# Performance work log

Measured on AMD Instinct MI355X. Metric: run time of the kernel, lower is better.

Reference implementation:

```python
import jax, jax.numpy as jnp
import numpy as np

N_NODES = 50000
N_EDGES = 800000
D_MODEL = 128
N_HEADS = 4
N_LAYERS = 2
F_HEAD = D_MODEL // N_HEADS


def setup_inputs() -> dict:
    key = jax.random.key(0)
    ks = jax.random.split(key, 6)
    x = jax.random.normal(ks[0], (N_NODES, D_MODEL), dtype=jnp.float32)
    edge_index = jax.random.randint(ks[1], (2, N_EDGES), 0, N_NODES, dtype=jnp.int64)
    scale = 1.0 / np.sqrt(D_MODEL)
    W = jax.random.normal(ks[2], (N_LAYERS, D_MODEL, D_MODEL), dtype=jnp.float32) * scale
    a_src = jax.random.normal(ks[3], (N_LAYERS, N_HEADS, F_HEAD), dtype=jnp.float32) * scale
    a_dst = jax.random.normal(ks[4], (N_LAYERS, N_HEADS, F_HEAD), dtype=jnp.float32) * scale
    b = jnp.zeros((N_LAYERS, D_MODEL), dtype=jnp.float32)
    return {"x": x, "edge_index": edge_index, "W": W, "a_src": a_src, "a_dst": a_dst, "b": b}


def _gat_layer(x, src, dst, W_l, a_src_l, a_dst_l, b_l, apply_act):
    N = x.shape[0]
    H, F = a_src_l.shape
    # projected node features, split into heads: [N, H, F]
    h = (x @ W_l).reshape(N, H, F)
    # per-node attention contributions: [N, H]
    alpha_s = jnp.einsum("nhf,hf->nh", h, a_src_l)
    alpha_d = jnp.einsum("nhf,hf->nh", h, a_dst_l)
    # per-edge raw scores, LeakyReLU(0.2): [E, H]
    e = jax.nn.leaky_relu(alpha_s[src] + alpha_d[dst], negative_slope=0.2)
    # numerically-stable segment softmax over edges grouped by target node
    e_max = jax.ops.segment_max(e, dst, num_segments=N)
    e_exp = jnp.exp(e - e_max[dst])
    denom = jax.ops.segment_sum(e_exp, dst, num_segments=N)
    alpha = e_exp / (denom[dst] + 1e-16)  # [E, H]
    # gather source features, weight, scatter-add to targets
    msg = h[src] * alpha[:, :, None]  # [E, H, F]
    out = jax.ops.segment_sum(msg, dst, num_segments=N).reshape(N, H * F)
    out = out + x + b_l  # skip connection (dims match) + bias
    return jax.nn.elu(out) if apply_act else out


def reference(x, edge_index, W, a_src, a_dst, b):
    src, dst = edge_index[0], edge_index[1]
    L = W.shape[0]
    for l in range(L):
        x = _gat_layer(x, src, dst, W[l], a_src[l], a_dst[l], b[l], apply_act=(l < L - 1))
    return x
```

## Files before the change

### kernel.cpp

```cpp
#include <hip/hip_runtime.h>
#include <math.h>

constexpr int NN = 50000;
constexpr int NE = 800000;
constexpr int D  = 128;
constexpr int NH = 4;
constexpr int NBUK = (NN + 255) / 256;
constexpr int CAP  = 4608;

typedef __attribute__((ext_vector_type(8))) short short8v;
typedef __attribute__((ext_vector_type(4))) float f32x4;

__device__ inline unsigned short rne_bf16(float f) {
    unsigned bits = __float_as_uint(f);
    return (unsigned short)((bits + 0x7FFFu + ((bits >> 16) & 1u)) >> 16);
}

__global__ __launch_bounds__(256) void partition_kernel(
    const int* __restrict__ src, const int* __restrict__ dst,
    int* __restrict__ bwp, unsigned* __restrict__ bukbuf)
{
    __shared__ int cnt[NBUK];
    __shared__ int run[NBUK];
    for (int i = threadIdx.x; i < NBUK; i += 256) cnt[i] = 0;
    __syncthreads();
    const int base = blockIdx.x * 2048;
    int s_[8], b_[8], dl_[8];
    #pragma unroll
    for (int i = 0; i < 8; ++i) {
        int e = base + i * 256 + threadIdx.x;
        bool ok = (e < NE);
        s_[i] = ok ? src[e] : 0;
        int d = ok ? dst[e] : 0;
        b_[i] = d >> 8; dl_[i] = d & 255;
        if (ok) atomicAdd(&cnt[b_[i]], 1);
    }
    __syncthreads();
    for (int i = threadIdx.x; i < NBUK; i += 256)
        run[i] = cnt[i] ? atomicAdd(&bwp[i], cnt[i]) : 0;
    __syncthreads();
    #pragma unroll
    for (int i = 0; i < 8; ++i) {
        int e = base + i * 256 + threadIdx.x;
        if (e < NE) {
            int pos = atomicAdd(&run[b_[i]], 1);
            if (pos < CAP)
                bukbuf[b_[i] * CAP + pos] = (unsigned)s_[i] | ((unsigned)dl_[i] << 16);
        }
    }
}

__global__ __launch_bounds__(256) void bucket_sort_kernel(
    const unsigned* __restrict__ bukbuf, const int* __restrict__ bwp,
    int* __restrict__ row_start, int* __restrict__ row_end,
    unsigned short* __restrict__ srcs)
{
    const int b = blockIdx.x;
    const int t = threadIdx.x;
    const int cnt = min(bwp[b], CAP);
    const int base = b * CAP;
    __shared__ int hist[256];
    __shared__ int run[256];
    __shared__ int s[256];
    __shared__ unsigned short stage[CAP];
    hist[t] = 0;
    __syncthreads();
    for (int i = t; i < cnt; i += 256)
        atomicAdd(&hist[bukbuf[base + i] >> 16], 1);
    __syncthreads();
    int v = hist[t];
    s[t] = v;
    __syncthreads();
    for (int off = 1; off < 256; off <<= 1) {
        int u = (t >= off) ? s[t - off] : 0;
        __syncthreads();
        s[t] += u;
        __syncthreads();
    }
    const int excl = s[t] - v;
    const int node = b * 256 + t;
    if (node < NN) {
        row_start[node] = base + excl;
        row_end[node]   = base + excl + v;
    }
    run[t] = excl;
    __syncthreads();
    for (int i = t; i < cnt; i += 256) {
        unsigned p = bukbuf[base + i];
        int pos = atomicAdd(&run[p >> 16], 1);
        stage[pos] = (unsigned short)(p & 0xFFFFu);
    }
    __syncthreads();
    for (int i = t; i < cnt; i += 256) srcs[base + i] = stage[i];
}

__global__ __launch_bounds__(256) void repack_kernel(const float* __restrict__ W,
                                                     unsigned short* __restrict__ Wpk,
                                                     int* __restrict__ bwp) {
    if (blockIdx.x == 0 && threadIdx.x < NBUK) bwp[threadIdx.x] = 0;
    int tid = blockIdx.x * 256 + threadIdx.x;
    if (tid >= 2 * 2048) return;
    int layer = tid >> 11;
    int rest  = tid & 2047;
    int tile  = rest >> 8;
    int kstep = (rest >> 6) & 3;
    int lane  = rest & 63;
    int col   = tile * 16 + (lane & 15);
    int kbase = kstep * 32 + (lane >> 4) * 8;
    const float* Wl = W + (size_t)layer * D * D;
    unsigned short v[8];
    #pragma unroll
    for (int j = 0; j < 8; ++j) v[j] = rne_bf16(Wl[(kbase + j) * D + col]);
    *(uint4*)(Wpk + (size_t)tid * 8) = *(const uint4*)v;
}

template<int BF16IN>
__global__ __launch_bounds__(256) void gemm_alpha_kernel(
    const void* __restrict__ xin, const unsigned short* __restrict__ Wpk,
    const float* __restrict__ a_src, const float* __restrict__ a_dst,
    unsigned short* __restrict__ hb, float* __restrict__ alpha_s,
    float* __restrict__ alpha_d)
{
    __shared__ unsigned short xl[64 * 128];
    const int t = threadIdx.x;
    const int row0 = blockIdx.x * 64;

    if constexpr (BF16IN) {
        const unsigned short* xb = (const unsigned short*)xin;
        #pragma unroll
        for (int it = 0; it < 4; ++it) {
            int idx = it * 256 + t;
            int r   = idx >> 4;
            int c8  = (idx & 15) * 8;
            int n   = row0 + r;
            uint4 v = {0u, 0u, 0u, 0u};
            if (n < NN) v = *(const uint4*)(xb + (size_t)n * D + c8);
            *(uint4*)(xl + r * 128 + (c8 ^ ((r & 7) << 3))) = v;
        }
    } else {
        const float* xf = (const float*)xin;
        #pragma unroll
        for (int it = 0; it < 8; ++it) {
            int idx = it * 256 + t;
            int r   = idx >> 5;
            int c4  = (idx & 31) * 4;
            int n   = row0 + r;
            float4 v;
            if (n < NN) v = *(const float4*)(xf + (size_t)n * D + c4);
            else { v.x = 0.f; v.y = 0.f; v.z = 0.f; v.w = 0.f; }
            unsigned p0 = ((unsigned)rne_bf16(v.y) << 16) | rne_bf16(v.x);
            unsigned p1 = ((unsigned)rne_bf16(v.w) << 16) | rne_bf16(v.z);
            uint2 pv; pv.x = p0; pv.y = p1;
            *(uint2*)(xl + r * 128 + (c4 ^ ((r & 7) << 3))) = pv;
        }
    }
    __syncthreads();

    const int wv  = t >> 6;
    const int l   = t & 63;
    const int l15 = l & 15;
    const int g   = l >> 4;
    const int strip = wv * 16;
    const int arow  = strip + l15;

    f32x4 acc[8];
    #pragma unroll
    for (int i = 0; i < 8; ++i) acc[i] = (f32x4){0.f, 0.f, 0.f, 0.f};

    #pragma unroll
    for (int ks = 0; ks < 4; ++ks) {
        const int k0 = ks * 32 + g * 8;
        short8v a = *(const short8v*)(xl + arow * 128 + (k0 ^ ((arow & 7) << 3)));
        #pragma unroll
        for (int tl = 0; tl < 8; ++tl) {
            short8v b = *(const short8v*)(Wpk + ((size_t)(tl * 4 + ks) * 64 + l) * 8);
            acc[tl] = __builtin_amdgcn_mfma_f32_16x16x32_bf16(a, b, acc[tl], 0, 0, 0);
        }
    }

    float as_t[8], ad_t[8];
    #pragma unroll
    for (int tl = 0; tl < 8; ++tl) {
        as_t[tl] = a_src[tl * 16 + l15];
        ad_t[tl] = a_dst[tl * 16 + l15];
    }

    #pragma unroll
    for (int r = 0; r < 4; ++r) {
        const int n = row0 + strip + g * 4 + r;
        if (n < NN) {
            #pragma unroll
            for (int tl = 0; tl < 8; ++tl)
                hb[(size_t)n * D + tl * 16 + l15] = rne_bf16(acc[tl][r]);
        }
        #pragma unroll
        for (int hd = 0; hd < NH; ++hd) {
            float ps = acc[2*hd][r] * as_t[2*hd] + acc[2*hd+1][r] * as_t[2*hd+1];
            float pd = acc[2*hd][r] * ad_t[2*hd] + acc[2*hd+1][r] * ad_t[2*hd+1];
            #pragma unroll
            for (int off = 1; off < 16; off <<= 1) {
                ps += __shfl_xor(ps, off);
                pd += __shfl_xor(pd, off);
            }
            if (l15 == 0 && n < NN) {
                alpha_s[n * NH + hd] = ps;
                alpha_d[n * NH + hd] = pd;
            }
        }
    }
}

template<int IN_BF16, int OUT_BF16, int ACT>
__global__ __launch_bounds__(256) void gather_kernel(
    const unsigned short* __restrict__ hb, const float* __restrict__ alpha_s,
    const float* __restrict__ alpha_d, const int* __restrict__ row_start,
    const int* __restrict__ row_end, const unsigned short* __restrict__ srcs,
    const void* __restrict__ x_in, const float* __restrict__ bias,
    void* __restrict__ out)
{
    const int lane = threadIdx.x & 63;
    const int q    = lane >> 4;
    const int ql   = lane & 15;
    const int head = ql >> 2;
    const int lb   = q * 16;
    const int n = blockIdx.x * 16 + (threadIdx.x >> 6) * 4 + q;
    if (n >= NN) return;

    const int start = row_start[n];
    const int end   = row_end[n];
    const float4 ad4 = *(const float4*)&alpha_d[n * NH];

    float acc[8];
    #pragma unroll
    for (int c = 0; c < 8; ++c) acc[c] = 0.f;
    float den = 0.f;

    for (int base = start; base < end; base += 16) {
        const int cnt = min(16, end - base);
        int msrc = 0;
        unsigned uw01 = 0, uw23 = 0;
        if (ql < cnt) {
            msrc = srcs[base + ql];
            const float4 as4 = *(const float4*)&alpha_s[msrc * NH];
            float e0 = as4.x + ad4.x; e0 = (e0 > 0.f) ? e0 : 0.2f * e0;
            float e1 = as4.y + ad4.y; e1 = (e1 > 0.f) ? e1 : 0.2f * e1;
            float e2 = as4.z + ad4.z; e2 = (e2 > 0.f) ? e2 : 0.2f * e2;
            float e3 = as4.w + ad4.w; e3 = (e3 > 0.f) ? e3 : 0.2f * e3;
            float w0 = __expf(e0), w1 = __expf(e1);
            float w2 = __expf(e2), w3 = __expf(e3);
            uw01 = ((unsigned)rne_bf16(w1) << 16) | rne_bf16(w0);
            uw23 = ((unsigned)rne_bf16(w3) << 16) | rne_bf16(w2);
        }
        for (int m = 0; m < cnt; ++m) {
            int s = __shfl(msrc, lb + m);
            unsigned b01 = (unsigned)__shfl((int)uw01, lb + m);
            unsigned b23 = (unsigned)__shfl((int)uw23, lb + m);
            unsigned uw = (head < 2) ? b01 : b23;
            float w = __uint_as_float((head & 1) ? (uw & 0xFFFF0000u) : (uw << 16));
            den += w;
            const uint4 hv = *(const uint4*)(hb + ((size_t)s << 7) + (ql << 3));
            acc[0] = fmaf(w, __uint_as_float(hv.x << 16),          acc[0]);
            acc[1] = fmaf(w, __uint_as_float(hv.x & 0xFFFF0000u),  acc[1]);
            acc[2] = fmaf(w, __uint_as_float(hv.y << 16),          acc[2]);
            acc[3] = fmaf(w, __uint_as_float(hv.y & 0xFFFF0000u),  acc[3]);
            acc[4] = fmaf(w, __uint_as_float(hv.z << 16),          acc[4]);
            acc[5] = fmaf(w, __uint_as_float(hv.z & 0xFFFF0000u),  acc[5]);
            acc[6] = fmaf(w, __uint_as_float(hv.w << 16),          acc[6]);
            acc[7] = fmaf(w, __uint_as_float(hv.w & 0xFFFF0000u),  acc[7]);
        }
    }

    const float inv = 1.f / (den + 1e-16f);
    const size_t o8 = (size_t)n * D + ql * 8;
    float xi[8];
    if constexpr (IN_BF16) {
        const uint4 xv = *(const uint4*)((const unsigned short*)x_in + o8);
        xi[0] = __uint_as_float(xv.x << 16);
        xi[1] = __uint_as_float(xv.x & 0xFFFF0000u);
        xi[2] = __uint_as_float(xv.y << 16);
        xi[3] = __uint_as_float(xv.y & 0xFFFF0000u);
        xi[4] = __uint_as_float(xv.z << 16);
        xi[5] = __uint_as_float(xv.z & 0xFFFF0000u);
        xi[6] = __uint_as_float(xv.w << 16);
        xi[7] = __uint_as_float(xv.w & 0xFFFF0000u);
    } else {
        const float4 a = *(const float4*)((const float*)x_in + o8);
        const float4 b = *(const float4*)((const float*)x_in + o8 + 4);
        xi[0]=a.x; xi[1]=a.y; xi[2]=a.z; xi[3]=a.w;
        xi[4]=b.x; xi[5]=b.y; xi[6]=b.z; xi[7]=b.w;
    }
    const float4 ba = *(const float4*)(bias + ql * 8);
    const float4 bb = *(const float4*)(bias + ql * 8 + 4);
    const float bi[8] = {ba.x, ba.y, ba.z, ba.w, bb.x, bb.y, bb.z, bb.w};
    float o[8];
    #pragma unroll
    for (int c = 0; c < 8; ++c) {
        float v = fmaf(acc[c], inv, xi[c]) + bi[c];
        if constexpr (ACT) v = (v > 0.f) ? v : (__expf(v) - 1.f);
        o[c] = v;
    }
    if constexpr (OUT_BF16) {
        unsigned short ov[8];
        #pragma unroll
        for (int c = 0; c < 8; ++c) ov[c] = rne_bf16(o[c]);
        *(uint4*)((unsigned short*)out + o8) = *(const uint4*)ov;
    } else {
        float4 oa = {o[0], o[1], o[2], o[3]};
        float4 ob = {o[4], o[5], o[6], o[7]};
        *(float4*)((float*)out + o8)     = oa;
        *(float4*)((float*)out + o8 + 4) = ob;
    }
}

extern "C" void kernel_launch(void* const* d_in, const int* in_sizes, int n_in,
                              void* d_out, int out_size, void* d_ws, size_t ws_size,
                              hipStream_t stream) {
    const float* x     = (const float*)d_in[0];
    const int*   ei    = (const int*)d_in[1];
    const float* W     = (const float*)d_in[2];
    const float* a_src = (const float*)d_in[3];
    const float* a_dst = (const float*)d_in[4];
    const float* bias  = (const float*)d_in[5];
    float* outp = (float*)d_out;

    const int* e_src = ei;
    const int* e_dst = ei + NE;

    char* base = (char*)d_ws;
    unsigned short* hb  = (unsigned short*)(base);
    unsigned short* x1b = (unsigned short*)(base + 12800000);
    float* al_s      = (float*)(base + 25600000);
    float* al_d      = (float*)(base + 26400000);
    int*   row_start = (int*)  (base + 27200000);
    int*   row_end   = (int*)  (base + 27400000);
    unsigned short* srcs = (unsigned short*)(base + 27600000);
    unsigned* bukbuf = (unsigned*)(base + 29406336);
    int*   bwp       = (int*)  (base + 33019008);
    unsigned short* Wpk = (unsigned short*)(base + 33019792);

    repack_kernel<<<16, 256, 0, stream>>>(W, Wpk, bwp);
    const int pblocks = (NE + 2047) / 2048;
    partition_kernel<<<pblocks, 256, 0, stream>>>(e_src, e_dst, bwp, bukbuf);
    bucket_sort_kernel<<<NBUK, 256, 0, stream>>>(bukbuf, bwp, row_start, row_end, srcs);

    const int gemm_blocks   = (NN + 63) / 64;
    const int gather_blocks = (NN + 15) / 16;

    gemm_alpha_kernel<0><<<gemm_blocks, 256, 0, stream>>>(x, Wpk, a_src, a_dst,
                                                          hb, al_s, al_d);
    gather_kernel<0, 1, 1><<<gather_blocks, 256, 0, stream>>>(
        hb, al_s, al_d, row_start, row_end, srcs, x, bias, x1b);
    gemm_alpha_kernel<1><<<gemm_blocks, 256, 0, stream>>>(x1b, Wpk + 2048 * 8,
                                                          a_src + D, a_dst + D,
                                                          hb, al_s, al_d);
    gather_kernel<1, 0, 0><<<gather_blocks, 256, 0, stream>>>(
        hb, al_s, al_d, row_start, row_end, srcs, x1b, bias + D, outp);
}
```

Before: 141.0 us.

## Fold attention vectors into weight matrix and use bf16 dot2 in gather

The per-head attention vectors a_src and a_dst are pre-multiplied into W during repack and stored as a ninth MFMA column tile. The GEMM then produces alpha_s and alpha_d directly, with no per-row shuffle reductions. The gather inner loop now handles two edges per step, packing their bf16 features and weights with perm and accumulating with v_dot2_f32_bf16, which roughly halves the FMA and unpack instruction count. The cost is one extra MFMA tile per k-step and some precision loss, since the folded W·a products are rounded to bf16 and the edge weights pass through bf16 dot products.

```diff
diff --git a/kernel.cpp b/kernel.cpp
--- a/kernel.cpp
+++ b/kernel.cpp
@@ -7,6 +7,7 @@
 constexpr int NH = 4;
 constexpr int NBUK = (NN + 255) / 256;
 constexpr int CAP  = 4608;
+constexpr int FR_PER_LAYER = 9 * 4 * 64;
 
 typedef __attribute__((ext_vector_type(8))) short short8v;
 typedef __attribute__((ext_vector_type(4))) float f32x4;
@@ -15,6 +16,9 @@
     unsigned bits = __float_as_uint(f);
     return (unsigned short)((bits + 0x7FFFu + ((bits >> 16) & 1u)) >> 16);
 }
+
+#define DOT2BF(accv, pa, pb) \
+    asm("v_dot2_f32_bf16 %0, %1, %2, %0" : "+v"(accv) : "v"(pa), "v"(pb))
 
 __global__ __launch_bounds__(256) void partition_kernel(
     const int* __restrict__ src, const int* __restrict__ dst,
@@ -94,30 +98,48 @@
     for (int i = t; i < cnt; i += 256) srcs[base + i] = stage[i];
 }
 
-__global__ __launch_bounds__(256) void repack_kernel(const float* __restrict__ W,
-                                                     unsigned short* __restrict__ Wpk,
-                                                     int* __restrict__ bwp) {
+__global__ __launch_bounds__(256) void repack_kernel(
+    const float* __restrict__ W, const float* __restrict__ a_src,
+    const float* __restrict__ a_dst, unsigned short* __restrict__ Wpk,
+    int* __restrict__ bwp)
+{
     if (blockIdx.x == 0 && threadIdx.x < NBUK) bwp[threadIdx.x] = 0;
     int tid = blockIdx.x * 256 + threadIdx.x;
-    if (tid >= 2 * 2048) return;
-    int layer = tid >> 11;
-    int rest  = tid & 2047;
+    if (tid >= 2 * FR_PER_LAYER) return;
+    int layer = tid / FR_PER_LAYER;
+    int rest  = tid % FR_PER_LAYER;
     int tile  = rest >> 8;
     int kstep = (rest >> 6) & 3;
     int lane  = rest & 63;
-    int col   = tile * 16 + (lane & 15);
+    int col   = lane & 15;
     int kbase = kstep * 32 + (lane >> 4) * 8;
     const float* Wl = W + (size_t)layer * D * D;
     unsigned short v[8];
-    #pragma unroll
-    for (int j = 0; j < 8; ++j) v[j] = rne_bf16(Wl[(kbase + j) * D + col]);
+    if (tile < 8) {
+        int c = tile * 16 + col;
+        #pragma unroll
+        for (int j = 0; j < 8; ++j) v[j] = rne_bf16(Wl[(kbase + j) * D + c]);
+    } else {
+        #pragma unroll
+        for (int j = 0; j < 8; ++j) v[j] = 0;
+        if (col < 8) {
+            const float* av = ((col < 4) ? a_src : a_dst) + layer * D + (col & 3) * 32;
+            const int hbase = (col & 3) * 32;
+            for (int j = 0; j < 8; ++j) {
+                float sum = 0.f;
+                const float* wr = Wl + (size_t)(kbase + j) * D + hbase;
+                #pragma unroll
+                for (int jj = 0; jj < 32; ++jj) sum = fmaf(wr[jj], av[jj], sum);
+                v[j] = rne_bf16(sum);
+            }
+        }
+    }
     *(uint4*)(Wpk + (size_t)tid * 8) = *(const uint4*)v;
 }
 
 template<int BF16IN>
 __global__ __launch_bounds__(256) void gemm_alpha_kernel(
     const void* __restrict__ xin, const unsigned short* __restrict__ Wpk,
-    const float* __restrict__ a_src, const float* __restrict__ a_dst,
     unsigned short* __restrict__ hb, float* __restrict__ alpha_s,
     float* __restrict__ alpha_d)
 {
@@ -163,26 +185,19 @@
     const int strip = wv * 16;
     const int arow  = strip + l15;
 
-    f32x4 acc[8];
-    #pragma unroll
-    for (int i = 0; i < 8; ++i) acc[i] = (f32x4){0.f, 0.f, 0.f, 0.f};
+    f32x4 acc[9];
+    #pragma unroll
+    for (int i = 0; i < 9; ++i) acc[i] = (f32x4){0.f, 0.f, 0.f, 0.f};
 
     #pragma unroll
     for (int ks = 0; ks < 4; ++ks) {
         const int k0 = ks * 32 + g * 8;
         short8v a = *(const short8v*)(xl + arow * 128 + (k0 ^ ((arow & 7) << 3)));
         #pragma unroll
-        for (int tl = 0; tl < 8; ++tl) {
+        for (int tl = 0; tl < 9; ++tl) {
             short8v b = *(const short8v*)(Wpk + ((size_t)(tl * 4 + ks) * 64 + l) * 8);
             acc[tl] = __builtin_amdgcn_mfma_f32_16x16x32_bf16(a, b, acc[tl], 0, 0, 0);
         }
-    }
-
-    float as_t[8], ad_t[8];
-    #pragma unroll
-    for (int tl = 0; tl < 8; ++tl) {
-        as_t[tl] = a_src[tl * 16 + l15];
-        ad_t[tl] = a_dst[tl * 16 + l15];
     }
 
     #pragma unroll
@@ -192,20 +207,9 @@
             #pragma unroll
             for (int tl = 0; tl < 8; ++tl)
                 hb[(size_t)n * D + tl * 16 + l15] = rne_bf16(acc[tl][r]);
-        }
-        #pragma unroll
-        for (int hd = 0; hd < NH; ++hd) {
-            float ps = acc[2*hd][r] * as_t[2*hd] + acc[2*hd+1][r] * as_t[2*hd+1];
-            float pd = acc[2*hd][r] * ad_t[2*hd] + acc[2*hd+1][r] * ad_t[2*hd+1];
-            #pragma unroll
-            for (int off = 1; off < 16; off <<= 1) {
-                ps += __shfl_xor(ps, off);
-                pd += __shfl_xor(pd, off);
-            }
-            if (l15 == 0 && n < NN) {
-                alpha_s[n * NH + hd] = ps;
-                alpha_d[n * NH + hd] = pd;
-            }
+            const float av = acc[8][r];
+            if (l15 < 4)      alpha_s[n * NH + l15]       = av;
+            else if (l15 < 8) alpha_d[n * NH + (l15 - 4)] = av;
         }
     }
 }
@@ -229,6 +233,8 @@
     const int start = row_start[n];
     const int end   = row_end[n];
     const float4 ad4 = *(const float4*)&alpha_d[n * NH];
+    const unsigned wsel = (head & 1) ? 0x07060302u : 0x05040100u;
+    const unsigned ones = 0x3F803F80u;
 
     float acc[8];
     #pragma unroll
@@ -251,22 +257,29 @@
             uw01 = ((unsigned)rne_bf16(w1) << 16) | rne_bf16(w0);
             uw23 = ((unsigned)rne_bf16(w3) << 16) | rne_bf16(w2);
         }
-        for (int m = 0; m < cnt; ++m) {
-            int s = __shfl(msrc, lb + m);
-            unsigned b01 = (unsigned)__shfl((int)uw01, lb + m);
-            unsigned b23 = (unsigned)__shfl((int)uw23, lb + m);
-            unsigned uw = (head < 2) ? b01 : b23;
-            float w = __uint_as_float((head & 1) ? (uw & 0xFFFF0000u) : (uw << 16));
-            den += w;
-            const uint4 hv = *(const uint4*)(hb + ((size_t)s << 7) + (ql << 3));
-            acc[0] = fmaf(w, __uint_as_float(hv.x << 16),          acc[0]);
-            acc[1] = fmaf(w, __uint_as_float(hv.x & 0xFFFF0000u),  acc[1]);
-            acc[2] = fmaf(w, __uint_as_float(hv.y << 16),          acc[2]);
-            acc[3] = fmaf(w, __uint_as_float(hv.y & 0xFFFF0000u),  acc[3]);
-            acc[4] = fmaf(w, __uint_as_float(hv.z << 16),          acc[4]);
-            acc[5] = fmaf(w, __uint_as_float(hv.z & 0xFFFF0000u),  acc[5]);
-            acc[6] = fmaf(w, __uint_as_float(hv.w << 16),          acc[6]);
-            acc[7] = fmaf(w, __uint_as_float(hv.w & 0xFFFF0000u),  acc[7]);
+        const int mm = (cnt + 1) & ~1;
+        for (int m = 0; m < mm; m += 2) {
+            int s0 = __shfl(msrc, lb + m);
+            int s1 = __shfl(msrc, lb + m + 1);
+            unsigned a01 = (unsigned)__shfl((int)uw01, lb + m);
+            unsigned a23 = (unsigned)__shfl((int)uw23, lb + m);
+            unsigned c01 = (unsigned)__shfl((int)uw01, lb + m + 1);
+            unsigned c23 = (unsigned)__shfl((int)uw23, lb + m + 1);
+            unsigned uwA = (head < 2) ? a01 : a23;
+            unsigned uwB = (head < 2) ? c01 : c23;
+            unsigned wpair = __builtin_amdgcn_perm(uwB, uwA, wsel);
+            DOT2BF(den, wpair, ones);
+            const uint4 h0 = *(const uint4*)(hb + ((size_t)s0 << 7) + (ql << 3));
+            const uint4 h1 = *(const uint4*)(hb + ((size_t)s1 << 7) + (ql << 3));
+            unsigned p;
+            p = __builtin_amdgcn_perm(h1.x, h0.x, 0x05040100u); DOT2BF(acc[0], p, wpair);
+            p = __builtin_amdgcn_perm(h1.x, h0.x, 0x07060302u); DOT2BF(acc[1], p, wpair);
+            p = __builtin_amdgcn_perm(h1.y, h0.y, 0x05040100u); DOT2BF(acc[2], p, wpair);
+            p = __builtin_amdgcn_perm(h1.y, h0.y, 0x07060302u); DOT2BF(acc[3], p, wpair);
+            p = __builtin_amdgcn_perm(h1.z, h0.z, 0x05040100u); DOT2BF(acc[4], p, wpair);
+            p = __builtin_amdgcn_perm(h1.z, h0.z, 0x07060302u); DOT2BF(acc[5], p, wpair);
+            p = __builtin_amdgcn_perm(h1.w, h0.w, 0x05040100u); DOT2BF(acc[6], p, wpair);
+            p = __builtin_amdgcn_perm(h1.w, h0.w, 0x07060302u); DOT2BF(acc[7], p, wpair);
         }
     }
 
@@ -338,7 +351,8 @@
     int*   bwp       = (int*)  (base + 33019008);
     unsigned short* Wpk = (unsigned short*)(base + 33019792);
 
-    repack_kernel<<<16, 256, 0, stream>>>(W, Wpk, bwp);
+    const int rblocks = (2 * FR_PER_LAYER + 255) / 256;
+    repack_kernel<<<rblocks, 256, 0, stream>>>(W, a_src, a_dst, Wpk, bwp);
     const int pblocks = (NE + 2047) / 2048;
     partition_kernel<<<pblocks, 256, 0, stream>>>(e_src, e_dst, bwp, bukbuf);
     bucket_sort_kernel<<<NBUK, 256, 0, stream>>>(bukbuf, bwp, row_start, row_end, srcs);
@@ -346,13 +360,11 @@
     const int gemm_blocks   = (NN + 63) / 64;
     const int gather_blocks = (NN + 15) / 16;
 
-    gemm_alpha_kernel<0><<<gemm_blocks, 256, 0, stream>>>(x, Wpk, a_src, a_dst,
-                                                          hb, al_s, al_d);
+    gemm_alpha_kernel<0><<<gemm_blocks, 256, 0, stream>>>(x, Wpk, hb, al_s, al_d);
     gather_kernel<0, 1, 1><<<gather_blocks, 256, 0, stream>>>(
         hb, al_s, al_d, row_start, row_end, srcs, x, bias, x1b);
-    gemm_alpha_kernel<1><<<gemm_blocks, 256, 0, stream>>>(x1b, Wpk + 2048 * 8,
-                                                          a_src + D, a_dst + D,
-                                                          hb, al_s, al_d);
+    gemm_alpha_kernel<1><<<gemm_blocks, 256, 0, stream>>>(
+        x1b, Wpk + (size_t)FR_PER_LAYER * 8, hb, al_s, al_d);
     gather_kernel<1, 0, 0><<<gather_blocks, 256, 0, stream>>>(
         hb, al_s, al_d, row_start, row_end, srcs, x1b, bias + D, outp);
 }
```

After: 133.5 us. 5.3% less time.
